# Performance work log

Hardware: AMD Instinct MI355X
Metric: run time of the kernel (lower is better)

The kernel has to match this reference:

```python
import jax, jax.numpy as jnp
import numpy as np


def setup_inputs() -> dict:
    B, L, D, M, S = 4, 1024, 1024, 16, 8
    key = jax.random.key(0)
    ks = jax.random.split(key, 12)
    sd = 0.02
    inp = {
        "hid": jax.random.normal(ks[0], (B, L, D), jnp.float32),
        "src_hid": jax.random.normal(ks[1], (B, L, D), jnp.float32),
        "sp_width": jax.random.randint(ks[2], (B, L), 0, 9),
        "max_sp_len": S,
        "attention_mask": jnp.ones((B, L), bool),
        "src_mask": jnp.ones((B, L), bool),
        # span-start attention (1 head): query/key linears + relative-key embedding table
        "wq_st": sd * jax.random.normal(ks[3], (D, D), jnp.float32),
        "bq_st": jnp.zeros((D,), jnp.float32),
        "wk_st": sd * jax.random.normal(ks[4], (D, D), jnp.float32),
        "bk_st": jnp.zeros((D,), jnp.float32),
        "rel_st": sd * jax.random.normal(ks[5], (2 * M + 1, D), jnp.float32),
        # span-end attention
        "wq_ed": sd * jax.random.normal(ks[6], (D, D), jnp.float32),
        "bq_ed": jnp.zeros((D,), jnp.float32),
        "wk_ed": sd * jax.random.normal(ks[7], (D, D), jnp.float32),
        "bk_ed": jnp.zeros((D,), jnp.float32),
        "rel_ed": sd * jax.random.normal(ks[8], (2 * M + 1, D), jnp.float32),
        # sp_emb: Linear(2D -> D), stored as [2D, D] (x @ W + b)
        "sp_w": sd * jax.random.normal(ks[9], (2 * D, D), jnp.float32),
        "sp_b": jnp.zeros((D,), jnp.float32),
    }
    return inp


def reference(hid, src_hid, sp_width, max_sp_len, attention_mask, src_mask,
              wq_st, bq_st, wk_st, bk_st, rel_st,
              wq_ed, bq_ed, wk_ed, bk_ed, rel_ed, sp_w, sp_b):
    B, L, D = hid.shape
    scale = 1.0 / jnp.sqrt(jnp.float32(D))
    M = (rel_st.shape[0] - 1) // 2
    pos = jnp.arange(L)
    rel_idx = jnp.clip(pos[None, :] - pos[:, None], -M, M) + M          # [L,L]
    rel_idx_b = jnp.broadcast_to(rel_idx[None], (B, L, L))

    amask = (src_mask[:, :, None] & attention_mask[:, None, :]).astype(jnp.float32)  # [B,Lq,Lk]
    attn_w0 = amask / jnp.clip(jnp.sum(amask, 2, keepdims=True), 1e-6)

    def attn(query, wq, bq, wk, bk, rel_tab, mask):
        # single-head relative-position attention; returns attention weights [B,L,L]
        q = (query @ wq + bq) * scale                                   # [B,L,D]
        k = hid @ wk + bk                                               # [B,L,D]
        sc = jnp.einsum('bqd,bkd->bqk', q, k)
        # q . rel_emb[rel_idx[q_pos,k_pos]]: contract with table then gather (avoids [L,L,D])
        rel_sc = jnp.take_along_axis(jnp.einsum('bqd,rd->bqr', q, rel_tab), rel_idx_b, axis=2)
        sc = jnp.where(mask > 0, sc + rel_sc, -1e18)
        return jax.nn.softmax(sc, axis=-1)

    def upd(attn_w, hidp):
        # weighted sum of hid + linear + relu (dropout is identity in eval)
        hidc = jnp.einsum('bqk,bkd->bqd', attn_w, hid)
        return jax.nn.relu(jnp.concatenate([hidp, hidc], axis=2) @ sp_w + sp_b)

    sts, eds, masks = [attn_w0], [attn_w0], []
    hid1, hid2 = src_hid, src_hid
    for i in range(max_sp_len):
        m = (i < sp_width).astype(jnp.float32)                          # [B,L]
        masks.append(m)
        mask_i = m[:, :, None] * amask                                  # [B,L,L]
        hid1 = upd(sts[-1], hid1)
        sts.append(attn(hid1, wq_st, bq_st, wk_st, bk_st, rel_st, mask_i))
        hid2 = upd(eds[-1], hid2)
        eds.append(attn(hid2, wq_ed, bq_ed, wk_ed, bk_ed, rel_ed, mask_i))

    return (jnp.stack(sts[1:], -2),   # [B,L,S,L]
            jnp.stack(eds[1:], -2),   # [B,L,S,L]
            jnp.stack(masks, -1))     # [B,L,S]
```

## Files before the change

### kernel.cpp

```cpp
#include <hip/hip_runtime.h>

typedef unsigned short u16;
typedef __attribute__((ext_vector_type(8))) short bh8;
typedef __attribute__((ext_vector_type(4))) float f4;

__device__ __forceinline__ u16 f2b(float x){
  union { float f; unsigned u; } c; c.f = x;
  unsigned r = (c.u + 0x7FFFu + ((c.u >> 16) & 1u)) >> 16;
  return (u16)r;
}
__device__ __forceinline__ float b2f(u16 h){
  union { unsigned u; float f; } c; c.u = ((unsigned)h) << 16; return c.f;
}
__device__ __forceinline__ void gload16(const void* g, void* l){
  __builtin_amdgcn_global_load_lds((const __attribute__((address_space(1))) void*)g,
                                   (__attribute__((address_space(3))) void*)l, 16, 0, 0);
}


__global__ __launch_bounds__(256) void convall_k(const float* __restrict__ hid,
                                                 const float* __restrict__ wq0, const float* __restrict__ wq1,
                                                 const float* __restrict__ wk0, const float* __restrict__ wk1,
                                                 u16* __restrict__ hidB, u16* __restrict__ wqB, u16* __restrict__ wkB){
  long i = (long)blockIdx.x*256 + threadIdx.x;
  const float* src; u16* dst; long off;
  if      (i < 4194304L){ src = hid; dst = hidB;           off = i; }
  else if (i < 5242880L){ src = wq0; dst = wqB;            off = i - 4194304L; }
  else if (i < 6291456L){ src = wq1; dst = wqB + 1048576;  off = i - 5242880L; }
  else if (i < 7340032L){ src = wk0; dst = wkB;            off = i - 6291456L; }
  else                  { src = wk1; dst = wkB + 1048576;  off = i - 7340032L; }
  dst[off] = f2b(src[off]);
}

__global__ __launch_bounds__(256) void uniform0_k(const int* __restrict__ spw, float* __restrict__ out){
  int bl = blockIdx.x;
  if (spw[bl] != 0) return;
  f4 t = {0.0009765625f, 0.0009765625f, 0.0009765625f, 0.0009765625f};
  float* b0 = out + (size_t)bl*8192;
  float* b1 = out + 33554432ull + (size_t)bl*8192;
  #pragma unroll
  for (int i = 0; i < 8; i++){
    ((f4*)(b0 + (size_t)i*1024))[threadIdx.x] = t;
    ((f4*)(b1 + (size_t)i*1024))[threadIdx.x] = t;
  }
}

__global__ __launch_bounds__(256) void trans_k(const float* __restrict__ in, u16* __restrict__ out,
                                               int R, int C){
  __shared__ u16 t[32][33];
  int bx = blockIdx.x*32, by = blockIdx.y*32;
  int tx = threadIdx.x & 31, ty = threadIdx.x >> 5;
  #pragma unroll
  for (int j = 0; j < 32; j += 8) t[ty+j][tx] = f2b(in[(size_t)(by+ty+j)*C + bx+tx]);
  __syncthreads();
  #pragma unroll
  for (int j = 0; j < 32; j += 8) out[(size_t)(bx+ty+j)*R + by+tx] = t[tx][ty+j];
}

__global__ __launch_bounds__(256) void sort_k(const int* __restrict__ spw, int* __restrict__ perm,
                                              int* __restrict__ cnt, float* __restrict__ mout){
  int b = blockIdx.x, t = threadIdx.x;
  __shared__ int hist[9], start[9];
  if (t < 9) hist[t] = 0;
  __syncthreads();
  for (int l = t; l < 1024; l += 256) atomicAdd(&hist[spw[b*1024 + l]], 1);
  __syncthreads();
  if (t == 0){
    int acc = 0;
    for (int w = 8; w >= 0; w--){ start[w] = acc; acc += hist[w]; }
  }
  __syncthreads();
  if (t < 8) cnt[b*8 + t] = start[t];
  __syncthreads();
  for (int l = t; l < 1024; l += 256){
    int w = spw[b*1024 + l];
    float* mo = mout + ((size_t)b*1024 + l)*8;
    #pragma unroll
    for (int i = 0; i < 8; i++) mo[i] = (i < w) ? 1.0f : 0.0f;
    int pos = atomicAdd(&start[w], 1);
    perm[b*1024 + pos] = l;
  }
}

__global__ __launch_bounds__(256) void gather_k(const float* __restrict__ srch, const int* __restrict__ perm,
                                                u16* __restrict__ hb){
  int blk = blockIdx.x;
  int z = blk >> 10, c = blk & 1023, b = z & 3;
  int ro = perm[b*1024 + c];
  const float* src = srch + ((size_t)b*1024 + ro)*1024;
  u16* dst = hb + ((size_t)z*1024 + c)*1024;
  for (int d = threadIdx.x; d < 1024; d += 256) dst[d] = f2b(src[d]);
}

__global__ __launch_bounds__(256) void wrt_k(const float* __restrict__ wq0, const float* __restrict__ wq1,
                                             const float* __restrict__ rel0, const float* __restrict__ rel1,
                                             u16* __restrict__ Mx){
  long idx = (long)blockIdx.x*256 + threadIdx.x;
  if (idx >= 2L*33*1024) return;
  int s = idx >= 33*1024; long loc = idx - (s ? 33*1024 : 0);
  int r = (int)(loc >> 10), e = (int)(loc & 1023);
  const float* wqrow = (s ? wq1 : wq0) + (size_t)e*1024;
  const float* rel = (s ? rel1 : rel0) + (size_t)r*1024;
  float acc = 0.0f;
  #pragma unroll 4
  for (int k = 0; k < 1024; k++) acc += wqrow[k]*rel[k];
  u16 v = f2b(acc*0.03125f);
  size_t o = (size_t)(1024 + r)*1024 + e;
  #pragma unroll
  for (int b = 0; b < 4; b++)
    Mx[(size_t)(s*4 + b)*1179648 + o] = v;
}

__global__ __launch_bounds__(256) void dots_k(const float* __restrict__ wq0, const float* __restrict__ wq1,
                                              const float* __restrict__ wk0, const float* __restrict__ wk1,
                                              const float* __restrict__ bq0, const float* __restrict__ bq1,
                                              const float* __restrict__ bk0, const float* __restrict__ bk1,
                                              const float* __restrict__ rel0, const float* __restrict__ rel1,
                                              float* __restrict__ ubuf, float* __restrict__ c0buf,
                                              float* __restrict__ bqbk, float* __restrict__ cba){
  int row = blockIdx.x*4 + (threadIdx.x >> 6);
  int lane = threadIdx.x & 63;
  if (row >= 4164) return;
  const float *a, *v;
  int kind = 0, oi = 0, br_s = 0, br_r = 0;
  if      (row < 1024){ a = wk0 + (size_t)row*1024; v = bq0; oi = row; }
  else if (row < 2048){ a = wk1 + (size_t)(row-1024)*1024; v = bq1; oi = row; }
  else if (row < 3072){ a = wq0 + (size_t)(row-2048)*1024; v = bk0; kind = 1; oi = row-2048; }
  else if (row < 4096){ a = wq1 + (size_t)(row-3072)*1024; v = bk1; kind = 1; oi = row-3072+1024; }
  else if (row < 4162){ int idx = row-4096; br_s = idx/33; br_r = idx%33;
                        a = (br_s ? rel1 : rel0) + (size_t)br_r*1024; v = br_s ? bq1 : bq0; kind = 2; }
  else                { int s2 = row-4162; a = s2 ? bq1 : bq0; v = s2 ? bk1 : bk0; kind = 3; oi = s2; }
  const f4* ap = (const f4*)a;
  const f4* vp = (const f4*)v;
  float acc = 0.0f;
  #pragma unroll
  for (int p = 0; p < 4; p++){
    f4 x = ap[lane + 64*p], y = vp[lane + 64*p];
    acc += x[0]*y[0] + x[1]*y[1] + x[2]*y[2] + x[3]*y[3];
  }
  #pragma unroll
  for (int off = 32; off > 0; off >>= 1) acc += __shfl_xor(acc, off, 64);
  if (lane == 0){
    if (kind == 0) ubuf[oi] = acc;
    else if (kind == 1) c0buf[oi] = acc;
    else if (kind == 2){
      float w = acc*0.03125f;
      for (int b = 0; b < 4; b++) cba[(br_s*4 + b)*1152 + 1024 + br_r] = w;
    } else bqbk[oi] = acc;
  }
}

__global__ __launch_bounds__(256) void cba_k(const float* __restrict__ hid, const float* __restrict__ u,
                                             const float* __restrict__ bqbk, float* __restrict__ cba){
  int row = blockIdx.x*4 + (threadIdx.x >> 6);
  int lane = threadIdx.x & 63;
  int z = row >> 10, l = row & 1023, b = z & 3, s = z >> 2;
  const f4* hp = (const f4*)(hid + ((size_t)b*1024 + l)*1024);
  const f4* up = (const f4*)(u + s*1024);
  float acc = 0.0f;
  #pragma unroll
  for (int p = 0; p < 4; p++){
    f4 a = hp[lane + 64*p], c = up[lane + 64*p];
    acc += a[0]*c[0] + a[1]*c[1] + a[2]*c[2] + a[3]*c[3];
  }
  #pragma unroll
  for (int off = 32; off > 0; off >>= 1) acc += __shfl_xor(acc, off, 64);
  if (!lane) cba[z*1152 + l] = (acc + bqbk[s])*0.03125f;
}

__global__ __launch_bounds__(256) void meanh2_k(const u16* __restrict__ H2T, float* __restrict__ mh){
  int row = blockIdx.x*4 + (threadIdx.x >> 6);
  int lane = threadIdx.x & 63;
  const u16* p = H2T + (size_t)row*1024 + lane*16;
  float s = 0.0f;
  #pragma unroll
  for (int j = 0; j < 16; j++) s += b2f(p[j]);
  #pragma unroll
  for (int off = 32; off > 0; off >>= 1) s += __shfl_xor(s, off, 64);
  if (lane == 0) mh[row] = s * 0.0009765625f;
}

__global__ __launch_bounds__(256) void softmax_k(const u16* __restrict__ scB, float* __restrict__ outF,
                                                 u16* __restrict__ attnP, const float* __restrict__ qrelb,
                                                 const int* __restrict__ cnt, const int* __restrict__ perm,
                                                 const int* __restrict__ spw, int iter){
  int z = blockIdx.x >> 10, c = blockIdx.x & 1023;
  int s = z >> 2, b = z & 3;
  if (c >= cnt[b*8 + iter]) return;
  int ro = perm[b*1024 + c];
  __shared__ float qr[33];
  __shared__ float red[8];
  if (threadIdx.x < 33) qr[threadIdx.x] = qrelb[((size_t)z*1024 + c)*33 + threadIdx.x];
  __syncthreads();
  const u16* sc = scB + ((size_t)z*1024 + c)*1024;
  float* po = outF + (size_t)s*33554432ull + (((size_t)(b*1024 + ro))*8 + (size_t)iter)*1024;
  u16* pr = attnP + ((size_t)z*1024 + c)*1024;
  int t = threadIdx.x;
  float v[4]; float mx = -1e30f;
  #pragma unroll
  for (int j = 0; j < 4; j++){
    int col = t + j*256;
    int d = col - ro; d = d < -16 ? -16 : (d > 16 ? 16 : d);
    v[j] = b2f(sc[col]) + qr[d + 16];
    mx = fmaxf(mx, v[j]);
  }
  #pragma unroll
  for (int off = 32; off > 0; off >>= 1) mx = fmaxf(mx, __shfl_xor(mx, off, 64));
  int wv = t >> 6, ln = t & 63;
  if (ln == 0) red[wv] = mx;
  __syncthreads();
  mx = fmaxf(fmaxf(red[0], red[1]), fmaxf(red[2], red[3]));
  float sm = 0.0f;
  #pragma unroll
  for (int j = 0; j < 4; j++){ v[j] = __expf(v[j] - mx); sm += v[j]; }
  #pragma unroll
  for (int off = 32; off > 0; off >>= 1) sm += __shfl_xor(sm, off, 64);
  if (ln == 0) red[4 + wv] = sm;
  __syncthreads();
  sm = red[4] + red[5] + red[6] + red[7];
  float inv = 1.0f / sm;
  #pragma unroll
  for (int j = 0; j < 4; j++){
    float pv = v[j] * inv;
    po[t + j*256] = pv;
    pr[t + j*256] = f2b(pv);
  }
  int w = spw[b*1024 + ro];
  if (iter == w - 1 && w < 8){
    f4 u = {0.0009765625f, 0.0009765625f, 0.0009765625f, 0.0009765625f};
    for (int j = 1; j <= 7 - iter; j++)
      ((f4*)(po + (size_t)j*1024))[t] = u;
  }
}

template<int MODE>
__global__ __launch_bounds__(256) void gemm_k(
    const u16* __restrict__ A_, const u16* __restrict__ B_,
    const u16* __restrict__ A2_, const u16* __restrict__ B2_,
    const float* __restrict__ e0, const float* __restrict__ e1,
    u16* __restrict__ outB, float* __restrict__ qrelb,
    const int* __restrict__ cnt, int iter)
{
  const int z = blockIdx.z;
  const int s = (MODE == 1) ? 0 : (z >> 2);
  const int b = (MODE == 1) ? z : (z & 3);
  const size_t LD = 1024*1024;
  const int bm = blockIdx.y*128, bn = blockIdx.x*128;

  int cntv = 1024;
  if constexpr (MODE == 2 || MODE == 4){
    cntv = cnt[b*8 + iter];
    if (bm >= cntv) return;
  }

  const u16 *A1, *B1, *A2, *B2;
  int lda1 = 1024, ldb1 = 1024, lda2 = 1024, ldb2 = 1024, K = 1024, K1 = 1024;

  if constexpr (MODE == 0){ A1 = A_ + (size_t)z*LD; B1 = B_ + (size_t)z*LD; A2=A1; B2=B1; }
  else if constexpr (MODE == 1){ A1 = A_ + 1024; lda1 = 2048; B1 = B_ + (size_t)z*LD; A2=A1; B2=B1; lda2=lda1; }
  else if constexpr (MODE == 2){
    A1 = A_ + (size_t)z*LD; B1 = B_ + (size_t)b*LD;
    A2 = A2_ + (size_t)z*LD; B2 = B2_; ldb2 = 2048;
    if (iter == 0){ K = 1024; K1 = 0; } else { K = 2048; K1 = 1024; }
  }
  else if constexpr (MODE == 3){ A1 = A_ + (size_t)b*LD; B1 = B_ + (size_t)s*LD; A2=A1; B2=B1; }
  else { A1 = A_ + (size_t)z*LD; B1 = B_ + (size_t)z*1179648; A2=A1; B2=B1; }

  __shared__ __align__(16) u16 lA[16384];
  __shared__ __align__(16) u16 lB[16384];
  const int tid = threadIdx.x, wv = tid >> 6, lane = tid & 63;
  const int wr = (wv >> 1)*64, wc = (wv & 1)*64;
  const int fr = lane & 15, kh = lane >> 4;
  const int stRow = (lane >> 2);
  const int ssw  = ((lane >> 2) & 3) ^ ((lane >> 4) & 3);
  const int stCe = ((lane & 3) ^ ssw)*8;
  const int fsw  = (fr & 3) ^ ((fr >> 2) & 3);
  const int rdSl = (kh ^ fsw)*8;

  auto stage = [&](int bufsel, int k0s){
    const u16 *As, *Bs; int kk, la, lb;
    if (k0s < K1){ As = A1; Bs = B1; kk = k0s; la = lda1; lb = ldb1; }
    else         { As = A2; Bs = B2; kk = k0s - K1; la = lda2; lb = ldb2; }
    #pragma unroll
    for (int c = 0; c < 4; c++){
      const int n = wv*4 + c;
      const int h = n >> 3;
      const int rl = (n & 7)*16 + stRow;
      const int ke = kk + h*32 + stCe;
      gload16(As + (size_t)(bm + rl)*la + ke, (char*)lA + bufsel*16384 + n*1024);
      gload16(Bs + (size_t)(bn + rl)*lb + ke, (char*)lB + bufsel*16384 + n*1024);
    }
  };

  f4 acc[4][4];
  #pragma unroll
  for (int i = 0; i < 4; i++)
    #pragma unroll
    for (int j = 0; j < 4; j++)
      acc[i][j] = f4{0.f, 0.f, 0.f, 0.f};

  stage(0, 0);
  stage(1, 64);

  int cur = 0;
  for (int k0 = 0; k0 < K; k0 += 64){
    if (k0 + 64 < K) asm volatile("s_waitcnt vmcnt(8)" ::: "memory");
    else             asm volatile("s_waitcnt vmcnt(0)" ::: "memory");
    __builtin_amdgcn_s_barrier();
    asm volatile("" ::: "memory");
    const u16* bufA = lA + cur*8192;
    const u16* bufB = lB + cur*8192;
    bh8 af[2][4], bfr[2][4];
    #pragma unroll
    for (int h = 0; h < 2; h++){
      #pragma unroll
      for (int i = 0; i < 4; i++){
        af[h][i]  = *(const bh8*)&bufA[h*4096 + (wr + i*16 + fr)*32 + rdSl];
        bfr[h][i] = *(const bh8*)&bufB[h*4096 + (wc + i*16 + fr)*32 + rdSl];
      }
    }
    if (k0 + 128 < K){
      asm volatile("s_waitcnt lgkmcnt(0)" ::: "memory");
      __builtin_amdgcn_sched_barrier(0);
      __builtin_amdgcn_s_barrier();
      asm volatile("" ::: "memory");
      stage(cur, k0 + 128);
    }
    __builtin_amdgcn_s_setprio(1);
    #pragma unroll
    for (int h = 0; h < 2; h++)
      #pragma unroll
      for (int i = 0; i < 4; i++)
        #pragma unroll
        for (int j = 0; j < 4; j++)
          acc[i][j] = __builtin_amdgcn_mfma_f32_16x16x32_bf16(af[h][i], bfr[h][j], acc[i][j], 0, 0, 0);
    __builtin_amdgcn_s_setprio(0);
    cur ^= 1;
  }

  const int rw = (lane >> 4)*4, cl = lane & 15;
  #pragma unroll
  for (int i = 0; i < 4; i++){
    #pragma unroll
    for (int r = 0; r < 4; r++){
      const int row = bm + wr + i*16 + rw + r;
      if constexpr (MODE == 2 || MODE == 4){ if (row >= cntv) continue; }
      #pragma unroll
      for (int j = 0; j < 4; j++){
        const int col = bn + wc + j*16 + cl;
        float v = acc[i][j][r];
        if constexpr (MODE == 0 || MODE == 1){
          outB[(size_t)z*LD + (size_t)row*1024 + col] = f2b(v);
        } else if constexpr (MODE == 2){
          v += e0[col];
          if (e1) v += e1[b*1024 + col];
          v = fmaxf(v, 0.0f);
          outB[(size_t)z*LD + (size_t)row*1024 + col] = f2b(v);
        } else if constexpr (MODE == 3){
          outB[(size_t)z*1179648 + (size_t)row*1024 + col] = f2b((v + e0[s*1024 + col])*0.03125f);
        } else {
          v += e0[z*1152 + col];
          if (col < 1024){
            outB[((size_t)z*1024 + row)*1024 + col] = f2b(v);
          } else {
            int rr = col - 1024;
            if (rr < 33) qrelb[((size_t)z*1024 + row)*33 + rr] = v;
          }
        }
      }
    }
  }
}


extern "C" void kernel_launch(void* const* d_in, const int* in_sizes, int n_in,
                              void* d_out, int out_size, void* d_ws, size_t ws_size,
                              hipStream_t stream)
{
  const float* hid    = (const float*)d_in[0];
  const float* srch   = (const float*)d_in[1];
  const int*   spw    = (const int*)d_in[2];
  const float* wq_st  = (const float*)d_in[6];
  const float* bq_st  = (const float*)d_in[7];
  const float* wk_st  = (const float*)d_in[8];
  const float* bk_st  = (const float*)d_in[9];
  const float* rel_st = (const float*)d_in[10];
  const float* wq_ed  = (const float*)d_in[11];
  const float* bq_ed  = (const float*)d_in[12];
  const float* wk_ed  = (const float*)d_in[13];
  const float* bk_ed  = (const float*)d_in[14];
  const float* rel_ed = (const float*)d_in[15];
  const float* sp_w   = (const float*)d_in[16];
  const float* sp_b   = (const float*)d_in[17];
  float* out = (float*)d_out;

  const size_t LD = 1024*1024;
  char* p = (char*)d_ws;
  u16* hidB  = (u16*)p; p += 4*LD*2;
  u16* wqB   = (u16*)p; p += 2*LD*2;
  u16* wkB   = (u16*)p; p += 2*LD*2;
  u16* spwT  = (u16*)p; p += 2*LD*2;
  u16* WT    = (u16*)p; p += 2*LD*2;
  u16* H2T   = (u16*)p; p += 4*LD*2;
  u16* Mx    = (u16*)p; p += 8ull*1179648*2;
  u16* attnP = (u16*)p; p += 8*LD*2;
  u16* hbufA = (u16*)p; p += 8*LD*2;
  u16* hbufB = (u16*)p; p += 8*LD*2;
  u16* scB   = (u16*)p; p += 8*LD*2;
  float* qrelb  = (float*)p; p += 8*1024*33*4;
  float* cba    = (float*)p; p += 8*1152*4;
  float* ubuf   = (float*)p; p += 2048*4;
  float* c0buf  = (float*)p; p += 2048*4;
  float* bqbk   = (float*)p; p += 64;
  float* meanH2 = (float*)p; p += 4*1024*4;
  int*   perm   = (int*)p;   p += 4*1024*4;
  int*   cnt    = (int*)p;   p += 1024;

  const dim3 t256(256);

  convall_k<<<32768, t256, 0, stream>>>(hid, wq_st, wq_ed, wk_st, wk_ed, hidB, wqB, wkB);
  sort_k<<<4, t256, 0, stream>>>(spw, perm, cnt, out + 67108864ull);
  gather_k<<<8192, t256, 0, stream>>>(srch, perm, hbufA);
  uniform0_k<<<4096, t256, 0, stream>>>(spw, out);
  trans_k<<<dim3(32,64), t256, 0, stream>>>(sp_w, spwT, 2048, 1024);
  wrt_k<<<264, t256, 0, stream>>>(wq_st, wq_ed, rel_st, rel_ed, Mx);
  dots_k<<<1041, t256, 0, stream>>>(wq_st, wq_ed, wk_st, wk_ed, bq_st, bq_ed, bk_st, bk_ed,
                                    rel_st, rel_ed, ubuf, c0buf, bqbk, cba);
  cba_k<<<2048, t256, 0, stream>>>(hid, ubuf, bqbk, cba);

  gemm_k<0><<<dim3(8,8,2), t256, 0, stream>>>(wqB, wkB, nullptr, nullptr, nullptr, nullptr,
                                              WT, nullptr, nullptr, 0);
  gemm_k<3><<<dim3(8,8,8), t256, 0, stream>>>(hidB, WT, nullptr, nullptr, c0buf, nullptr,
                                              Mx, nullptr, nullptr, 0);
  gemm_k<1><<<dim3(8,8,4), t256, 0, stream>>>(spwT, hidB, nullptr, nullptr, nullptr, nullptr,
                                              H2T, nullptr, nullptr, 0);
  meanh2_k<<<1024, t256, 0, stream>>>(H2T, meanH2);

  u16* hp = hbufA; u16* hn = hbufB;
  for (int i = 0; i < 8; i++){
    gemm_k<2><<<dim3(8,8,8), t256, 0, stream>>>(attnP, H2T, hp, spwT, sp_b,
                                                (i == 0) ? meanH2 : nullptr,
                                                hn, nullptr, cnt, i);
    gemm_k<4><<<dim3(9,8,8), t256, 0, stream>>>(hn, Mx, nullptr, nullptr, cba, nullptr,
                                                scB, qrelb, cnt, i);
    softmax_k<<<8192, t256, 0, stream>>>(scB, out, attnP, qrelb, cnt, perm, spw, i);
    u16* tmp = hp; hp = hn; hn = tmp;
  }
}
```

Measured before the change: 919.1 us.

## Dedupe identical st/ed initial hidden states and merge precompute GEMMs

```diff
diff --git a/kernel.cpp b/kernel.cpp
--- a/kernel.cpp
+++ b/kernel.cpp
@@ -85,9 +85,9 @@
 __global__ __launch_bounds__(256) void gather_k(const float* __restrict__ srch, const int* __restrict__ perm,
                                                 u16* __restrict__ hb){
   int blk = blockIdx.x;
-  int z = blk >> 10, c = blk & 1023, b = z & 3;
-  int ro = perm[b*1024 + c];
-  const float* src = srch + ((size_t)b*1024 + ro)*1024;
+  int z = blk >> 10, c = blk & 1023;
+  int ro = perm[z*1024 + c];
+  const float* src = srch + ((size_t)z*1024 + ro)*1024;
   u16* dst = hb + ((size_t)z*1024 + c)*1024;
   for (int d = threadIdx.x; d < 1024; d += 256) dst[d] = f2b(src[d]);
 }
@@ -238,14 +238,15 @@
     const u16* __restrict__ A_, const u16* __restrict__ B_,
     const u16* __restrict__ A2_, const u16* __restrict__ B2_,
     const float* __restrict__ e0, const float* __restrict__ e1,
-    u16* __restrict__ outB, float* __restrict__ qrelb,
-    const int* __restrict__ cnt, int iter)
+    u16* __restrict__ outB, u16* __restrict__ outB2, float* __restrict__ qrelb,
+    const int* __restrict__ cnt, int iter, int azmask)
 {
   const int z = blockIdx.z;
-  const int s = (MODE == 1) ? 0 : (z >> 2);
-  const int b = (MODE == 1) ? z : (z & 3);
   const size_t LD = 1024*1024;
   const int bm = blockIdx.y*128, bn = blockIdx.x*128;
+  int s = z >> 2, b = z & 3;
+  bool m5h2 = false;
+  if constexpr (MODE == 5){ if (z >= 8){ m5h2 = true; b = z - 8; s = 0; } }
 
   int cntv = 1024;
   if constexpr (MODE == 2 || MODE == 4){
@@ -257,14 +258,17 @@
   int lda1 = 1024, ldb1 = 1024, lda2 = 1024, ldb2 = 1024, K = 1024, K1 = 1024;
 
   if constexpr (MODE == 0){ A1 = A_ + (size_t)z*LD; B1 = B_ + (size_t)z*LD; A2=A1; B2=B1; }
-  else if constexpr (MODE == 1){ A1 = A_ + 1024; lda1 = 2048; B1 = B_ + (size_t)z*LD; A2=A1; B2=B1; lda2=lda1; }
   else if constexpr (MODE == 2){
     A1 = A_ + (size_t)z*LD; B1 = B_ + (size_t)b*LD;
-    A2 = A2_ + (size_t)z*LD; B2 = B2_; ldb2 = 2048;
+    A2 = A2_ + (size_t)(z & azmask)*LD; B2 = B2_; ldb2 = 2048;
     if (iter == 0){ K = 1024; K1 = 0; } else { K = 2048; K1 = 1024; }
   }
-  else if constexpr (MODE == 3){ A1 = A_ + (size_t)b*LD; B1 = B_ + (size_t)s*LD; A2=A1; B2=B1; }
-  else { A1 = A_ + (size_t)z*LD; B1 = B_ + (size_t)z*1179648; A2=A1; B2=B1; }
+  else if constexpr (MODE == 4){ A1 = A_ + (size_t)(z & azmask)*LD; B1 = B_ + (size_t)z*1179648; A2=A1; B2=B1; }
+  else {
+    if (!m5h2){ A1 = A_ + (size_t)b*LD; B1 = B_ + (size_t)s*LD; }
+    else      { A1 = A2_ + 1024; lda1 = 2048; B1 = B2_ + (size_t)b*LD; }
+    A2=A1; B2=B1; lda2=lda1;
+  }
 
   __shared__ __align__(16) u16 lA[16384];
   __shared__ __align__(16) u16 lB[16384];
@@ -349,15 +353,18 @@
       for (int j = 0; j < 4; j++){
         const int col = bn + wc + j*16 + cl;
         float v = acc[i][j][r];
-        if constexpr (MODE == 0 || MODE == 1){
+        if constexpr (MODE == 0){
           outB[(size_t)z*LD + (size_t)row*1024 + col] = f2b(v);
         } else if constexpr (MODE == 2){
           v += e0[col];
           if (e1) v += e1[b*1024 + col];
           v = fmaxf(v, 0.0f);
           outB[(size_t)z*LD + (size_t)row*1024 + col] = f2b(v);
-        } else if constexpr (MODE == 3){
-          outB[(size_t)z*1179648 + (size_t)row*1024 + col] = f2b((v + e0[s*1024 + col])*0.03125f);
+        } else if constexpr (MODE == 5){
+          if (!m5h2)
+            outB[(size_t)z*1179648 + (size_t)row*1024 + col] = f2b((v + e0[s*1024 + col])*0.03125f);
+          else
+            outB2[(size_t)b*LD + (size_t)row*1024 + col] = f2b(v);
         } else {
           v += e0[z*1152 + col];
           if (col < 1024){
@@ -420,7 +427,7 @@
 
   convall_k<<<32768, t256, 0, stream>>>(hid, wq_st, wq_ed, wk_st, wk_ed, hidB, wqB, wkB);
   sort_k<<<4, t256, 0, stream>>>(spw, perm, cnt, out + 67108864ull);
-  gather_k<<<8192, t256, 0, stream>>>(srch, perm, hbufA);
+  gather_k<<<4096, t256, 0, stream>>>(srch, perm, hbufA);
   uniform0_k<<<4096, t256, 0, stream>>>(spw, out);
   trans_k<<<dim3(32,64), t256, 0, stream>>>(sp_w, spwT, 2048, 1024);
   wrt_k<<<264, t256, 0, stream>>>(wq_st, wq_ed, rel_st, rel_ed, Mx);
@@ -429,20 +436,21 @@
   cba_k<<<2048, t256, 0, stream>>>(hid, ubuf, bqbk, cba);
 
   gemm_k<0><<<dim3(8,8,2), t256, 0, stream>>>(wqB, wkB, nullptr, nullptr, nullptr, nullptr,
-                                              WT, nullptr, nullptr, 0);
-  gemm_k<3><<<dim3(8,8,8), t256, 0, stream>>>(hidB, WT, nullptr, nullptr, c0buf, nullptr,
-                                              Mx, nullptr, nullptr, 0);
-  gemm_k<1><<<dim3(8,8,4), t256, 0, stream>>>(spwT, hidB, nullptr, nullptr, nullptr, nullptr,
-                                              H2T, nullptr, nullptr, 0);
+                                              WT, nullptr, nullptr, nullptr, 0, 7);
+  gemm_k<5><<<dim3(8,8,12), t256, 0, stream>>>(hidB, WT, spwT, hidB, c0buf, nullptr,
+                                               Mx, H2T, nullptr, nullptr, 0, 7);
   meanh2_k<<<1024, t256, 0, stream>>>(H2T, meanH2);
 
   u16* hp = hbufA; u16* hn = hbufB;
   for (int i = 0; i < 8; i++){
-    gemm_k<2><<<dim3(8,8,8), t256, 0, stream>>>(attnP, H2T, hp, spwT, sp_b,
-                                                (i == 0) ? meanH2 : nullptr,
-                                                hn, nullptr, cnt, i);
+    int g2z = (i == 0) ? 4 : 8;
+    int am2 = (i <= 1) ? 3 : 7;
+    gemm_k<2><<<dim3(8,8,g2z), t256, 0, stream>>>(attnP, H2T, hp, spwT, sp_b,
+                                                  (i == 0) ? meanH2 : nullptr,
+                                                  hn, nullptr, nullptr, cnt, i, am2);
+    int am4 = (i == 0) ? 3 : 7;
     gemm_k<4><<<dim3(9,8,8), t256, 0, stream>>>(hn, Mx, nullptr, nullptr, cba, nullptr,
-                                                scB, qrelb, cnt, i);
+                                                scB, nullptr, qrelb, cnt, i, am4);
     softmax_k<<<8192, t256, 0, stream>>>(scB, out, attnP, qrelb, cnt, perm, spw, i);
     u16* tmp = hp; hp = hn; hn = tmp;
   }
```

Result: no change. 909.0 us (-1.1%).
